# Kernel tuning notes

Measured on AMD Instinct MI355X. Metric: run time of the kernel, lower is better.

## Reference

```python
import jax, jax.numpy as jnp
import numpy as np

B, L = 32, 96
N = B * L
E = B * L * L
HID, LAT, EEMB = 128, 64, 32
NLAYERS = 3
LAMBDA_CONTRAST = 0.05


def _sinusoidal(t, dim):
    half = dim // 2
    freqs = jnp.exp(-jnp.log(10000.0) * jnp.arange(half, dtype=jnp.float32) / (half - 1))
    ang = t[:, None] * freqs[None, :]
    return jnp.concatenate([jnp.sin(ang), jnp.cos(ang)], axis=-1)


def _forward(H_0, X_0, H_1, X_1, cond_embedding, t_graph,
             Wi1, bi1, Wi2, bi2, Wi3, bi3, edge_table,
             We1, be1, We2, be2, Wx, Wh1, bh1, Wh2, bh2, Wout, bout,
             edges, chain_ids, generate_mask, lengths, shift):
    n = H_0.shape[0]
    b = lengths.shape[0]
    batch_ids = jnp.repeat(jnp.arange(b), lengths, total_repeat_length=n)
    t = t_graph[batch_ids]                      # (N,)
    mask = generate_mask
    mask_f = mask.astype(jnp.float32)

    # path interpolation
    tH = t[:, None]
    H_t = jnp.where(mask[:, None], (1.0 - tH) * H_0 + tH * H_1, H_1)
    X_t = jnp.where(mask[:, None], (1.0 - tH) * X_0 + tH * X_1, X_1)
    v_H_target = H_1 - H_0
    v_X_target = X_1 - X_0

    # edge types from chain-id masking (irregular gather)
    row, col = edges[0], edges[1]
    edge_types = (chain_ids[row] != chain_ids[col]).astype(jnp.int32)

    # --- velocity net ---
    t_embed = _sinusoidal(t, HID)
    h = jnp.concatenate([H_t, cond_embedding, t_embed], axis=-1)
    h = jax.nn.relu(h @ Wi1 + bi1)
    h = jax.nn.relu(h @ Wi2 + bi2)
    h = h @ Wi3 + bi3                            # (N, HID)
    eemb = edge_table[edge_types]                # (E, EEMB)

    X = X_t
    for l in range(NLAYERS):
        rel = X[row] - X[col]                    # (E, 3)
        d2 = jnp.sum(rel * rel, axis=-1, keepdims=True)
        ef = jnp.concatenate([h[row], h[col], d2, eemb], axis=-1)
        m = jax.nn.silu(ef @ We1[l] + be1[l])
        m = jax.nn.silu(m @ We2[l] + be2[l])     # (E, HID)
        coef = m @ Wx[l]                         # (E, 1)
        X = X + jax.ops.segment_sum(rel * coef, row, num_segments=n)
        agg = jax.ops.segment_sum(m, row, num_segments=n)
        hh = jnp.concatenate([h, agg], axis=-1)
        h = h + jax.nn.silu(hh @ Wh1[l] + bh1[l]) @ Wh2[l] + bh2[l]

    v_X_pred = jnp.where(mask[:, None], X, 0.0)
    v_H_pred = jnp.where(mask[:, None], h @ Wout + bout, 0.0)

    # --- losses ---
    msum = mask_f.sum() + 1e-8
    def masked_mse(pred, tgt):
        return (jnp.sum((pred - tgt) ** 2, axis=-1) * mask_f).sum() / msum
    loss_H_pos = masked_mse(v_H_pred, v_H_target)
    loss_X_pos = masked_mse(v_X_pred, v_X_target)

    # negatives: roll over node dim (matches torch indexing (arange+shift)%N)
    v_H_target_neg = jnp.roll(H_1, -shift, axis=0) - jnp.roll(H_0, -shift, axis=0)
    v_X_target_neg = jnp.roll(X_1, -shift, axis=0) - jnp.roll(X_0, -shift, axis=0)
    loss_H_neg = masked_mse(v_H_pred, v_H_target_neg)
    loss_X_neg = masked_mse(v_X_pred, v_X_target_neg)

    loss_H = loss_H_pos - LAMBDA_CONTRAST * loss_H_neg
    loss_X = loss_X_pos - LAMBDA_CONTRAST * loss_X_neg
    return jnp.stack([loss_H, loss_X, loss_H_pos, loss_X_pos, loss_H_neg, loss_X_neg])


def setup_inputs() -> dict:
    key = jax.random.key(0)
    ks = iter(jax.random.split(key, 40))
    def nrm(shape, fan_in):
        return jax.random.normal(next(ks), shape, dtype=jnp.float32) / np.sqrt(fan_in)

    # all-pairs edges within each graph (uniform lengths)
    idx = np.arange(L)
    rb, cb = np.repeat(idx, L), np.tile(idx, L)
    off = (np.arange(B) * L)[:, None]
    rows = (off + rb[None, :]).reshape(-1)
    cols = (off + cb[None, :]).reshape(-1)
    edges = jnp.asarray(np.stack([rows, cols]).astype(np.int32))

    d_in_mlp = LAT + 2 * HID       # 320
    d_in_e = 2 * HID + 1 + EEMB    # 289
    inp = {
        "H_0": jax.random.normal(next(ks), (N, LAT), dtype=jnp.float32),
        "X_0": jax.random.normal(next(ks), (N, 3), dtype=jnp.float32),
        "H_1": jax.random.normal(next(ks), (N, LAT), dtype=jnp.float32),
        "X_1": jax.random.normal(next(ks), (N, 3), dtype=jnp.float32),
        "cond_embedding": jax.random.normal(next(ks), (N, HID), dtype=jnp.float32),
        "t_graph": jax.random.uniform(next(ks), (B,), dtype=jnp.float32),
        "Wi1": nrm((d_in_mlp, HID), d_in_mlp), "bi1": jnp.zeros((HID,)),
        "Wi2": nrm((HID, HID), HID), "bi2": jnp.zeros((HID,)),
        "Wi3": nrm((HID, HID), HID), "bi3": jnp.zeros((HID,)),
        "edge_table": jax.random.normal(next(ks), (2, EEMB), dtype=jnp.float32),
        "We1": nrm((NLAYERS, d_in_e, HID), d_in_e), "be1": jnp.zeros((NLAYERS, HID)),
        "We2": nrm((NLAYERS, HID, HID), HID), "be2": jnp.zeros((NLAYERS, HID)),
        "Wx": nrm((NLAYERS, HID, 1), HID) * 0.01,
        "Wh1": nrm((NLAYERS, 2 * HID, HID), 2 * HID), "bh1": jnp.zeros((NLAYERS, HID)),
        "Wh2": nrm((NLAYERS, HID, HID), HID), "bh2": jnp.zeros((NLAYERS, HID)),
        "Wout": nrm((HID, LAT), HID), "bout": jnp.zeros((LAT,)),
        "edges": edges,
        "chain_ids": jax.random.randint(next(ks), (N,), 0, 3).astype(jnp.int32),
        "generate_mask": jax.random.bernoulli(next(ks), 0.5, (N,)),
        "lengths": jnp.full((B,), L, dtype=jnp.int32),
        "shift": 7,
    }
    return inp


def reference(H_0, X_0, H_1, X_1, cond_embedding, t_graph,
              Wi1, bi1, Wi2, bi2, Wi3, bi3, edge_table,
              We1, be1, We2, be2, Wx, Wh1, bh1, Wh2, bh2, Wout, bout,
              edges, chain_ids, generate_mask, lengths, shift):
    return _forward(H_0, X_0, H_1, X_1, cond_embedding, t_graph,
                    Wi1, bi1, Wi2, bi2, Wi3, bi3, edge_table,
                    We1, be1, We2, be2, Wx, Wh1, bh1, Wh2, bh2, Wout, bout,
                    edges, chain_ids, generate_mask, lengths, shift)
```

## Files before the change

### kernel.cpp

```cpp
#include <hip/hip_runtime.h>
#include <hip/hip_bf16.h>
#include <math.h>

#define NBATCH 32
#define LSEQ   96
#define NN     3072
#define HID    128
#define LAT    64
#define EEMB   32

#define OFF_H      0
#define OFF_X      (OFF_H   + NN*HID)
#define OFF_PA     (OFF_X   + NN*3)
#define OFF_AGG    (OFF_PA  + NN*HID)
#define OFF_DX     (OFF_AGG + NN*HID)
#define OFF_ET     (OFF_DX  + NN*3)
#define OFF_ACC    (OFF_ET  + 768)
#define OFF_NBID   (OFF_ACC + 8)
#define OFF_CUM    (OFF_NBID + NN)
#define OFF_PBH    (OFF_CUM + 40)
#define OFF_BPE    (OFF_PBH + NN*HID/2)
#define OFF_BAB    (OFF_BPE + 24576)
#define OFF_BH1    (OFF_BAB + 49152)
#define OFF_BH2    (OFF_BH1 + 49152)
#define OFF_BWO    (OFF_BH2 + 24576)
#define OFF_BWI1   (OFF_BWO + 4096)
#define OFF_BWI2   (OFF_BWI1 + 20480)
#define OFF_BWI3   (OFF_BWI2 + 8192)

typedef short bf16x8 __attribute__((ext_vector_type(8)));
typedef float f32x4  __attribute__((ext_vector_type(4)));

__device__ __forceinline__ short f2bf(float f) {
    unsigned u = __builtin_bit_cast(unsigned, f);
    unsigned r = (u + 0x7FFFu + ((u >> 16) & 1u)) >> 16;
    return (short)r;
}
__device__ __forceinline__ short2 f2bf2(float a, float b) {
    __hip_bfloat162 h = __float22bfloat162_rn(make_float2(a, b));
    short2 r;
    __builtin_memcpy(&r, &h, sizeof(r));
    return r;
}
__device__ __forceinline__ float bf2f(short s) {
    unsigned u = ((unsigned)(unsigned short)s) << 16;
    return __builtin_bit_cast(float, u);
}
__device__ __forceinline__ float silu(float z) {
    return z * __builtin_amdgcn_rcpf(1.0f + __expf(-z));
}

__global__ void k0a_prep(const float* __restrict__ edge_table,
                         const float* __restrict__ We1,
                         const int* __restrict__ lengths,
                         float* __restrict__ ws) {
    int* cum = (int*)(ws + OFF_CUM);
    int* nb  = (int*)(ws + OFF_NBID);
    float* et = ws + OFF_ET;
    int tid = threadIdx.x;
    if (tid == 0) {
        int s = 0;
        for (int b = 0; b < NBATCH; b++) { cum[b] = s; s += lengths[b]; }
        cum[NBATCH] = s;
    }
    if (tid < 8) ws[OFF_ACC + tid] = 0.0f;
    __syncthreads();
    for (int i = tid; i < NN; i += blockDim.x) {
        int b = NBATCH - 1;
        for (int q = 0; q < NBATCH; q++) { if (i < cum[q + 1]) { b = q; break; } }
        nb[i] = b;
    }
    for (int idx = tid; idx < 3 * 2 * HID; idx += blockDim.x) {
        int c = idx & 127;
        int t = (idx >> 7) & 1;
        int l = idx >> 8;
        const float* w = We1 + (l * 289 + 257) * HID + c;
        const float* e = edge_table + t * EEMB;
        float s = 0.f;
        for (int k = 0; k < EEMB; k++) s += e[k] * w[k * HID];
        et[idx] = s;
    }
}

__global__ void k0b_transpose(const float* __restrict__ We1, const float* __restrict__ We2,
                              const float* __restrict__ Wh1, const float* __restrict__ Wh2,
                              const float* __restrict__ Wout, const float* __restrict__ Wi1,
                              const float* __restrict__ Wi2, const float* __restrict__ Wi3,
                              float* __restrict__ ws) {
    int idx = blockIdx.x * 256 + threadIdx.x;
    short* bpe  = (short*)(ws + OFF_BPE);
    short* bab  = (short*)(ws + OFF_BAB);
    short* bh1  = (short*)(ws + OFF_BH1);
    short* bh2  = (short*)(ws + OFF_BH2);
    short* bwo  = (short*)(ws + OFF_BWO);
    short* bwi1 = (short*)(ws + OFF_BWI1);
    short* bwi2 = (short*)(ws + OFF_BWI2);
    short* bwi3 = (short*)(ws + OFF_BWI3);
    if (idx < 49152) {
        int k = idx & 127, n = (idx >> 7) & 127, l = idx >> 14;
        bpe[idx] = f2bf(We2[(l * 128 + k) * 128 + n]);
    } else if (idx < 147456) {
        int q = idx - 49152;
        int k = q & 127, n = (q >> 7) & 255, l = q >> 15;
        float v = (n < 128) ? We1[(l * 289 + k) * 128 + n]
                            : We1[(l * 289 + 128 + k) * 128 + (n - 128)];
        bab[q] = f2bf(v);
    } else if (idx < 245760) {
        int q = idx - 147456;
        int k = q & 255, n = (q >> 8) & 127, l = q >> 15;
        bh1[q] = f2bf(Wh1[(l * 256 + k) * 128 + n]);
    } else if (idx < 294912) {
        int q = idx - 245760;
        int k = q & 127, n = (q >> 7) & 127, l = q >> 14;
        bh2[q] = f2bf(Wh2[(l * 128 + k) * 128 + n]);
    } else if (idx < 303104) {
        int q = idx - 294912;
        int k = q & 127, n = q >> 7;
        bwo[q] = f2bf(Wout[k * 64 + n]);
    } else if (idx < 344064) {
        int q = idx - 303104;
        int n = q / 320, k = q - n * 320;
        bwi1[q] = f2bf(Wi1[k * 128 + n]);
    } else if (idx < 360448) {
        int q = idx - 344064;
        int k = q & 127, n = q >> 7;
        bwi2[q] = f2bf(Wi2[k * 128 + n]);
    } else if (idx < 376832) {
        int q = idx - 360448;
        int k = q & 127, n = q >> 7;
        bwi3[q] = f2bf(Wi3[k * 128 + n]);
    }
}

__global__ void __launch_bounds__(256)
k1s_node_init(const float* __restrict__ H0, const float* __restrict__ X0,
              const float* __restrict__ H1, const float* __restrict__ X1,
              const float* __restrict__ cond, const float* __restrict__ tg,
              const float* __restrict__ bi1, const float* __restrict__ bi2,
              const float* __restrict__ bi3, const float* __restrict__ be1,
              const int* __restrict__ gmask, float* __restrict__ ws) {
    __shared__ short u1[16 * 136];
    __shared__ short u2[16 * 136];
// ... 104 lines not shown
        #pragma unroll
        for (int i = 0; i < 2; i++) {
            int ct = 2 * w + i;
            bf16x8 bf = *(const bf16x8*)(bwi3 + (size_t)(16 * ct + lp) * 128 + kb);
            acc[i] = __builtin_amdgcn_mfma_f32_16x16x32_bf16(af, bf, acc[i], 0, 0, 0);
        }
    }
    #pragma unroll
    for (int i = 0; i < 2; i++) {
        int ch = 16 * (2 * w + i) + lp;
        float bb3 = bi3[ch];
        #pragma unroll
        for (int r = 0; r < 4; r++) {
            int row = quad * 4 + r;
            float h = acc[i][r] + bb3;
            ws[OFF_H + (size_t)(rowbase + row) * 128 + ch] = h;
            u1[row * 136 + ch] = f2bf(h);
        }
    }
    __syncthreads();

    f32x4 acc4[4];
    #pragma unroll
    for (int i = 0; i < 4; i++) acc4[i] = (f32x4){0.f, 0.f, 0.f, 0.f};
    #pragma unroll
    for (int s = 0; s < 4; s++) {
        int kb = s * 32 + quad * 8;
        bf16x8 af = *(const bf16x8*)(u1 + lp * 136 + kb);
        #pragma unroll
        for (int i = 0; i < 4; i++) {
            int ct4 = 4 * w + i;
            bf16x8 bf = *(const bf16x8*)(bab + (size_t)(16 * ct4 + lp) * 128 + kb);
            acc4[i] = __builtin_amdgcn_mfma_f32_16x16x32_bf16(af, bf, acc4[i], 0, 0, 0);
        }
    }
    short* pbh = (short*)(ws + OFF_PBH);
    #pragma unroll
    for (int i = 0; i < 4; i++) {
        int ct4 = 4 * w + i;
        #pragma unroll
        for (int r = 0; r < 4; r++) {
            int node = rowbase + quad * 4 + r;
            if (ct4 < 8) {
                int ch = 16 * ct4 + lp;
                ws[OFF_PA + (size_t)node * 128 + ch] = acc4[i][r] + be1[ch];
            } else {
                int ch = 16 * (ct4 - 8) + lp;
                pbh[(size_t)node * 128 + ch] = f2bf(acc4[i][r]);
            }
        }
    }
}

#define KG 4
__global__ void __launch_bounds__(384)
k3_edge(const float* __restrict__ We1, const float* __restrict__ Wx,
        const float* __restrict__ be2, const int* __restrict__ chain,
        int l, float* __restrict__ ws) {
    __shared__ short bS[128 * 136];
    __shared__ float pe0S[KG * 128], pe1S[KG * 128];
    __shared__ float d2S[KG * 96];
    __shared__ int   selS[KG * 96];
    __shared__ float xS[96 * 3];
    __shared__ float xT[KG * 3];
    __shared__ float wcS[128], wxS[128], be2S[128];
    __shared__ float aggP[6 * 128];
    __shared__ float coefS[96];

    int tid = threadIdx.x;
    int i0 = blockIdx.x * KG;
    int colbase = (i0 / 96) * 96;
    const float* Xc = ws + OFF_X;

    {
        const short* bpe = (const short*)(ws + OFF_BPE) + (size_t)l * 128 * 128;
        for (int idx = tid; idx < 2048; idx += 384) {
            int row = idx >> 4, c = idx & 15;
            *(bf16x8*)(bS + row * 136 + c * 8) = *(const bf16x8*)(bpe + row * 128 + c * 8);
        }
        if (tid < 288) xS[tid] = Xc[colbase * 3 + tid];
        if (tid < KG * 3) xT[tid] = Xc[(size_t)(i0 + tid / 3) * 3 + tid % 3];
    }
    __syncthreads();

    if (tid < 128) {
        #pragma unroll
        for (int g = 0; g < KG; g++) {
            float pav = ws[OFF_PA + (size_t)(i0 + g) * 128 + tid];
            pe0S[g * 128 + tid] = pav + ws[OFF_ET + l * 256 + tid];
            pe1S[g * 128 + tid] = pav + ws[OFF_ET + l * 256 + 128 + tid];
        }
    } else if (tid < 224) {
        int j = tid - 128;
        int cj = chain[colbase + j];
        #pragma unroll
        for (int g = 0; g < KG; g++) {
            float rx = xT[g * 3 + 0] - xS[j * 3 + 0];
            float ry = xT[g * 3 + 1] - xS[j * 3 + 1];
            float rz = xT[g * 3 + 2] - xS[j * 3 + 2];
            d2S[g * 96 + j]  = rx * rx + ry * ry + rz * rz;
            selS[g * 96 + j] = (chain[i0 + g] != cj) ? 1 : 0;
        }
    } else if (tid < 352) {
        int c = tid - 224;
        wcS[c]  = We1[(l * 289 + 256) * 128 + c];
        wxS[c]  = Wx[l * 128 + c];
        be2S[c] = be2[l * 128 + c];
    }

    int w = tid >> 6, lane = tid & 63;
    int quad = lane >> 4, lp = lane & 15;
    int jA = 16 * w + lp;
    const short* pbrow = (const short*)(ws + OFF_PBH) + (size_t)(colbase + jA) * 128;
    bf16x8 pbv[4];
    #pragma unroll
    for (int s = 0; s < 4; s++) pbv[s] = *(const bf16x8*)(pbrow + s * 32 + quad * 8);
    __syncthreads();

    for (int g = 0; g < KG; g++) {
        float d2j = d2S[g * 96 + jA];
        const float* peB = (selS[g * 96 + jA] ? pe1S : pe0S) + g * 128;

        f32x4 acc[8];
        #pragma unroll
        for (int t = 0; t < 8; t++) acc[t] = (f32x4){0.f, 0.f, 0.f, 0.f};

        #pragma unroll
        for (int s = 0; s < 4; s++) {
            int kb = s * 32 + quad * 8;
            float z[8];
            #pragma unroll
            for (int e = 0; e < 8; e++)
                z[e] = silu(peB[kb + e] + bf2f(pbv[s][e]) + d2j * wcS[kb + e]);
            bf16x8 af;
            #pragma unroll
            for (int e = 0; e < 8; e += 2) {
                short2 p = f2bf2(z[e], z[e + 1]);
                af[e] = p.x; af[e + 1] = p.y;
            }
            #pragma unroll
            for (int t = 0; t < 8; t++) {
                bf16x8 bf = *(const bf16x8*)(bS + (16 * t + lp) * 136 + kb);
                acc[t] = __builtin_amdgcn_mfma_f32_16x16x32_bf16(af, bf, acc[t], 0, 0, 0);
            }
        }

        float cp[4] = {0.f, 0.f, 0.f, 0.f};
        #pragma unroll
        for (int t = 0; t < 8; t++) {
            int ch = 16 * t + lp;
            float bb = be2S[ch];
            float wx = wxS[ch];
            float ag = 0.f;
            #pragma unroll
            for (int r = 0; r < 4; r++) {
                float m2 = silu(acc[t][r] + bb);
                ag += m2;
                cp[r] += m2 * wx;
            }
            ag += __shfl_xor(ag, 16);
            ag += __shfl_xor(ag, 32);
            if (lane < 16) aggP[w * 128 + ch] = ag;
        }
        #pragma unroll
        for (int r = 0; r < 4; r++) {
            float v = cp[r];
            v += __shfl_xor(v, 1);
            v += __shfl_xor(v, 2);
            v += __shfl_xor(v, 4);
            v += __shfl_xor(v, 8);
            if (lp == 0) coefS[16 * w + quad * 4 + r] = v;
        }
        __syncthreads();

        if (tid < 128) {
            float s = 0.f;
            #pragma unroll
            for (int q = 0; q < 6; q++) s += aggP[q * 128 + tid];
            ws[OFF_AGG + (size_t)(i0 + g) * 128 + tid] = s;
        }
        if (w < 3) {
            float v = (xT[g * 3 + w] - xS[lane * 3 + w]) * coefS[lane];
            if (lane < 32) v += (xT[g * 3 + w] - xS[(lane + 64) * 3 + w]) * coefS[lane + 64];
            #pragma unroll
            for (int o = 32; o > 0; o >>= 1) v += __shfl_down(v, o);
            if (lane == 0) ws[OFF_DX + (size_t)(i0 + g) * 3 + w] = v;
        }
        if (g < KG - 1) __syncthreads();
    }
}

__global__ void __launch_bounds__(256)
k4s_node_post(const float* __restrict__ bh1, const float* __restrict__ bh2,
              const float* __restrict__ be1, const float* __restrict__ bout,
              const float* __restrict__ H0, const float* __restrict__ X0,
              const float* __restrict__ H1, const float* __restrict__ X1,
              const int* __restrict__ gmask, const int* __restrict__ shiftp,
              int l, float* __restrict__ ws) {
    __shared__ short uS[16 * 136];
    __shared__ short hS[16 * 136];
    __shared__ float redE[4], redN[4];
    __shared__ float sxp, sxn, scnt;
    int rowbase = blockIdx.x * 96 + blockIdx.y * 16;
    int tid = threadIdx.x;
    int w = tid >> 6, lane = tid & 63;
    int quad = lane >> 4, lp = lane & 15;
    int nodeA = rowbase + lp;
    const short* b1 = (const short*)(ws + OFF_BH1) + (size_t)l * 128 * 256;
    const short* b2 = (const short*)(ws + OFF_BH2) + (size_t)l * 128 * 128;

    if (tid == 0) { sxp = 0.f; sxn = 0.f; scnt = 0.f; }
    if (tid < 48) {
        int node = rowbase + tid / 3, d = tid % 3;
        ws[OFF_X + (size_t)node * 3 + d] += ws[OFF_DX + (size_t)node * 3 + d];
    }

    f32x4 acc[2];
    acc[0] = (f32x4){0.f, 0.f, 0.f, 0.f};
    acc[1] = (f32x4){0.f, 0.f, 0.f, 0.f};
    #pragma unroll
    for (int s = 0; s < 8; s++) {
        int kb = s * 32 + quad * 8;
        const float* src = (kb < 128) ? (ws + OFF_H + (size_t)nodeA * 128 + kb)
                                      : (ws + OFF_AGG + (size_t)nodeA * 128 + (kb - 128));
        bf16x8 af;
        #pragma unroll
        for (int e = 0; e < 8; e += 2) {
            short2 p = f2bf2(src[e], src[e + 1]);
            af[e] = p.x; af[e + 1] = p.y;
        }
        #pragma unroll
        for (int i = 0; i < 2; i++) {
            int ct = 2 * w + i;
            bf16x8 bf = *(const bf16x8*)(b1 + (size_t)(16 * ct + lp) * 256 + kb);
            acc[i] = __builtin_amdgcn_mfma_f32_16x16x32_bf16(af, bf, acc[i], 0, 0, 0);
        }
    }
    #pragma unroll
    for (int i = 0; i < 2; i++) {
        int ch = 16 * (2 * w + i) + lp;
        float bb1 = bh1[l * 128 + ch];
        #pragma unroll
        for (int r = 0; r < 4; r++)
            uS[(quad * 4 + r) * 136 + ch] = f2bf(silu(acc[i][r] + bb1));
    }
    __syncthreads();

    acc[0] = (f32x4){0.f, 0.f, 0.f, 0.f};
    acc[1] = (f32x4){0.f, 0.f, 0.f, 0.f};
    #pragma unroll
    for (int s = 0; s < 4; s++) {
        int kb = s * 32 + quad * 8;
        bf16x8 af = *(const bf16x8*)(uS + lp * 136 + kb);
        #pragma unroll
        for (int i = 0; i < 2; i++) {
            int ct = 2 * w + i;
            bf16x8 bf = *(const bf16x8*)(b2 + (size_t)(16 * ct + lp) * 128 + kb);
            acc[i] = __builtin_amdgcn_mfma_f32_16x16x32_bf16(af, bf, acc[i], 0, 0, 0);
        }
    }
    #pragma unroll
    for (int i = 0; i < 2; i++) {
        int ch = 16 * (2 * w + i) + lp;
        float bb2 = bh2[l * 128 + ch];
        #pragma unroll
        for (int r = 0; r < 4; r++) {
            int row = quad * 4 + r;
            size_t off = OFF_H + (size_t)(rowbase + row) * 128 + ch;
            float h = ws[off] + acc[i][r] + bb2;
            ws[off] = h;
            hS[row * 136 + ch] = f2bf(h);
        }
    }
    __syncthreads();

    if (l < 2) {
        const short* bab = (const short*)(ws + OFF_BAB) + (size_t)(l + 1) * 256 * 128;
        f32x4 acc4[4];
        #pragma unroll
        for (int i = 0; i < 4; i++) acc4[i] = (f32x4){0.f, 0.f, 0.f, 0.f};
        #pragma unroll
        for (int s = 0; s < 4; s++) {
            int kb = s * 32 + quad * 8;
            bf16x8 af = *(const bf16x8*)(hS + lp * 136 + kb);
            #pragma unroll
            for (int i = 0; i < 4; i++) {
                int ct4 = 4 * w + i;
                bf16x8 bf = *(const bf16x8*)(bab + (size_t)(16 * ct4 + lp) * 128 + kb);
                acc4[i] = __builtin_amdgcn_mfma_f32_16x16x32_bf16(af, bf, acc4[i], 0, 0, 0);
            }
        }
        short* pbh = (short*)(ws + OFF_PBH);
        #pragma unroll
        for (int i = 0; i < 4; i++) {
            int ct4 = 4 * w + i;
            #pragma unroll
            for (int r = 0; r < 4; r++) {
                int node = rowbase + quad * 4 + r;
                if (ct4 < 8) {
                    int ch = 16 * ct4 + lp;
                    ws[OFF_PA + (size_t)node * 128 + ch] = acc4[i][r] + be1[(l + 1) * 128 + ch];
                } else {
                    int ch = 16 * (ct4 - 8) + lp;
                    pbh[(size_t)node * 128 + ch] = f2bf(acc4[i][r]);
                }
            }
        }
    } else {
        const short* bwo = (const short*)(ws + OFF_BWO);
        f32x4 accv = (f32x4){0.f, 0.f, 0.f, 0.f};
        #pragma unroll
        for (int s = 0; s < 4; s++) {
            int kb = s * 32 + quad * 8;
            bf16x8 af = *(const bf16x8*)(hS + lp * 136 + kb);
            bf16x8 bf = *(const bf16x8*)(bwo + (size_t)(16 * w + lp) * 128 + kb);
            accv = __builtin_amdgcn_mfma_f32_16x16x32_bf16(af, bf, accv, 0, 0, 0);
        }
        int s = shiftp[0] % NN; if (s < 0) s += NN;
        int col = 16 * w + lp;
        float bo = bout[col];
        float ep = 0.f, en = 0.f;
        #pragma unroll
        for (int r = 0; r < 4; r++) {
            int row = rowbase + quad * 4 + r;
            if (gmask[row] != 0) {
                int ip = row + s; if (ip >= NN) ip -= NN;
                float v  = accv[r] + bo;
                float tp = H1[(size_t)row * 64 + col] - H0[(size_t)row * 64 + col];
                float tn = H1[(size_t)ip * 64 + col]  - H0[(size_t)ip * 64 + col];
                float dp = v - tp, dn = v - tn;
                ep += dp * dp;
                en += dn * dn;
            }
        }
        #pragma unroll
        for (int o = 1; o < 64; o <<= 1) {
            ep += __shfl_xor(ep, o);
            en += __shfl_xor(en, o);
        }
        if (lane == 0) { redE[w] = ep; redN[w] = en; }

        if (tid < 16) {
            int node = rowbase + tid;
            if (gmask[node] != 0) {
                int ip = node + s; if (ip >= NN) ip -= NN;
                float xp = 0.f, xn = 0.f;
                #pragma unroll
                for (int d = 0; d < 3; d++) {
                    float xv  = ws[OFF_X + (size_t)node * 3 + d];
                    float tpx = X1[(size_t)node * 3 + d] - X0[(size_t)node * 3 + d];
                    float tnx = X1[(size_t)ip * 3 + d]   - X0[(size_t)ip * 3 + d];
                    xp += (xv - tpx) * (xv - tpx);
                    xn += (xv - tnx) * (xv - tnx);
                }
                atomicAdd(&sxp, xp);
                atomicAdd(&sxn, xn);
                atomicAdd(&scnt, 1.0f);
            }
        }
        __syncthreads();
        if (tid == 0) {
            float eT = redE[0] + redE[1] + redE[2] + redE[3];
            float nT = redN[0] + redN[1] + redN[2] + redN[3];
            float* acc0 = ws + OFF_ACC;
            atomicAdd(acc0 + 0, eT);
            atomicAdd(acc0 + 2, nT);
            atomicAdd(acc0 + 1, sxp);
            atomicAdd(acc0 + 3, sxn);
            atomicAdd(acc0 + 4, scnt);
        }
    }
}

__global__ void k6_final(const float* __restrict__ ws, float* __restrict__ out) {
    if (threadIdx.x == 0) {
        const float* acc = ws + OFF_ACC;
        float msum = acc[4] + 1e-8f;
        float lhp = acc[0] / msum, lxp = acc[1] / msum;
        float lhn = acc[2] / msum, lxn = acc[3] / msum;
        out[0] = lhp - 0.05f * lhn;
        out[1] = lxp - 0.05f * lxn;
        out[2] = lhp;
        out[3] = lxp;
        out[4] = lhn;
        out[5] = lxn;
    }
}

extern "C" void kernel_launch(void* const* d_in, const int* in_sizes, int n_in,
                              void* d_out, int out_size, void* d_ws, size_t ws_size,
                              hipStream_t stream) {
    (void)in_sizes; (void)n_in; (void)out_size; (void)ws_size;
    const float* H0   = (const float*)d_in[0];
    const float* X0   = (const float*)d_in[1];
    const float* H1   = (const float*)d_in[2];
    const float* X1   = (const float*)d_in[3];
    const float* cond = (const float*)d_in[4];
    const float* tg   = (const float*)d_in[5];
    const float* Wi1  = (const float*)d_in[6];
    const float* bi1  = (const float*)d_in[7];
    const float* Wi2  = (const float*)d_in[8];
    const float* bi2  = (const float*)d_in[9];
    const float* Wi3  = (const float*)d_in[10];
    const float* bi3  = (const float*)d_in[11];
    const float* etab = (const float*)d_in[12];
    const float* We1  = (const float*)d_in[13];
    const float* be1  = (const float*)d_in[14];
    const float* We2  = (const float*)d_in[15];
    const float* be2  = (const float*)d_in[16];
    const float* Wx   = (const float*)d_in[17];
    const float* Wh1  = (const float*)d_in[18];
    const float* bh1  = (const float*)d_in[19];
    const float* Wh2  = (const float*)d_in[20];
    const float* bh2  = (const float*)d_in[21];
    const float* Wout = (const float*)d_in[22];
    const float* bout = (const float*)d_in[23];
    const int* chain   = (const int*)d_in[25];
    const int* gmask   = (const int*)d_in[26];
    const int* lengths = (const int*)d_in[27];
    const int* shiftp  = (const int*)d_in[28];
    float* ws  = (float*)d_ws;
    float* out = (float*)d_out;

    k0a_prep<<<1, 256, 0, stream>>>(etab, We1, lengths, ws);
    k0b_transpose<<<1472, 256, 0, stream>>>(We1, We2, Wh1, Wh2, Wout, Wi1, Wi2, Wi3, ws);
    k1s_node_init<<<dim3(NBATCH, 6), 256, 0, stream>>>(H0, X0, H1, X1, cond, tg,
                                                       bi1, bi2, bi3, be1, gmask, ws);
    for (int l = 0; l < 3; l++) {
        k3_edge<<<NN / KG, 384, 0, stream>>>(We1, Wx, be2, chain, l, ws);
        k4s_node_post<<<dim3(NBATCH, 6), 256, 0, stream>>>(bh1, bh2, be1, bout,
                                                           H0, X0, H1, X1, gmask, shiftp, l, ws);
    }
    k6_final<<<1, 64, 0, stream>>>(ws, out);
}
```

Baseline: 390.5 us.

## Fuse node-update into edge kernel via last-block-done counter; merge prep kernels

Merges the two prep kernels into one launch and fuses the per-layer node post-processing into the edge kernel. Each of the 24 blocks covering a 96-node graph bumps a global counter, and the last one to finish runs the node MLP update for the whole graph. This removes three kernel launches and the gaps between them. In exchange, the node work runs on only 32 blocks placed at the tail of each edge launch, so it is less parallel, and the atomic counter and threadfences add synchronisation cost.

```diff
diff --git a/kernel.cpp b/kernel.cpp
--- a/kernel.cpp
+++ b/kernel.cpp
@@ -27,6 +27,7 @@
 #define OFF_BWI1   (OFF_BWO + 4096)
 #define OFF_BWI2   (OFF_BWI1 + 20480)
 #define OFF_BWI3   (OFF_BWI2 + 8192)
+#define OFF_CNT    (OFF_BWI3 + 8192)
 
 typedef short bf16x8 __attribute__((ext_vector_type(8)));
 typedef float f32x4  __attribute__((ext_vector_type(4)));
@@ -50,44 +51,43 @@
     return z * __builtin_amdgcn_rcpf(1.0f + __expf(-z));
 }
 
-__global__ void k0a_prep(const float* __restrict__ edge_table,
-                         const float* __restrict__ We1,
-                         const int* __restrict__ lengths,
-                         float* __restrict__ ws) {
-    int* cum = (int*)(ws + OFF_CUM);
-    int* nb  = (int*)(ws + OFF_NBID);
-    float* et = ws + OFF_ET;
+__global__ void k0_all(const float* __restrict__ edge_table, const float* __restrict__ We1,
+                       const int* __restrict__ lengths, const float* __restrict__ We2,
+                       const float* __restrict__ Wh1, const float* __restrict__ Wh2,
+                       const float* __restrict__ Wout, const float* __restrict__ Wi1,
+                       const float* __restrict__ Wi2, const float* __restrict__ Wi3,
+                       float* __restrict__ ws) {
     int tid = threadIdx.x;
-    if (tid == 0) {
-        int s = 0;
-        for (int b = 0; b < NBATCH; b++) { cum[b] = s; s += lengths[b]; }
-        cum[NBATCH] = s;
-    }
-    if (tid < 8) ws[OFF_ACC + tid] = 0.0f;
-    __syncthreads();
-    for (int i = tid; i < NN; i += blockDim.x) {
-        int b = NBATCH - 1;
-        for (int q = 0; q < NBATCH; q++) { if (i < cum[q + 1]) { b = q; break; } }
-        nb[i] = b;
-    }
-    for (int idx = tid; idx < 3 * 2 * HID; idx += blockDim.x) {
-        int c = idx & 127;
-        int t = (idx >> 7) & 1;
-        int l = idx >> 8;
-        const float* w = We1 + (l * 289 + 257) * HID + c;
-        const float* e = edge_table + t * EEMB;
-        float s = 0.f;
-        for (int k = 0; k < EEMB; k++) s += e[k] * w[k * HID];
-        et[idx] = s;
-    }
-}
-
-__global__ void k0b_transpose(const float* __restrict__ We1, const float* __restrict__ We2,
-                              const float* __restrict__ Wh1, const float* __restrict__ Wh2,
-                              const float* __restrict__ Wout, const float* __restrict__ Wi1,
-                              const float* __restrict__ Wi2, const float* __restrict__ Wi3,
-                              float* __restrict__ ws) {
-    int idx = blockIdx.x * 256 + threadIdx.x;
+    if (blockIdx.x == 1472) {
+        int* cum = (int*)(ws + OFF_CUM);
+        int* nb  = (int*)(ws + OFF_NBID);
+        float* et = ws + OFF_ET;
+        if (tid == 0) {
+            int s = 0;
+            for (int b = 0; b < NBATCH; b++) { cum[b] = s; s += lengths[b]; }
+            cum[NBATCH] = s;
+        }
+        if (tid < 8) ws[OFF_ACC + tid] = 0.0f;
+        if (tid < 96) ((unsigned*)(ws + OFF_CNT))[tid] = 0u;
+        __syncthreads();
+        for (int i = tid; i < NN; i += blockDim.x) {
+            int b = NBATCH - 1;
+            for (int q = 0; q < NBATCH; q++) { if (i < cum[q + 1]) { b = q; break; } }
+            nb[i] = b;
+        }
+        for (int idx = tid; idx < 3 * 2 * HID; idx += blockDim.x) {
+            int c = idx & 127;
+            int t = (idx >> 7) & 1;
+            int l = idx >> 8;
+            const float* w = We1 + (l * 289 + 257) * HID + c;
+            const float* e = edge_table + t * EEMB;
+            float s = 0.f;
+            for (int k = 0; k < EEMB; k++) s += e[k] * w[k * HID];
+            et[idx] = s;
+        }
+        return;
+    }
+    int idx = blockIdx.x * 256 + tid;
     short* bpe  = (short*)(ws + OFF_BPE);
     short* bab  = (short*)(ws + OFF_BAB);
     short* bh1  = (short*)(ws + OFF_BH1);
@@ -299,23 +299,47 @@
 }
 
 #define KG 4
-__global__ void __launch_bounds__(384)
-k3_edge(const float* __restrict__ We1, const float* __restrict__ Wx,
-        const float* __restrict__ be2, const int* __restrict__ chain,
-        int l, float* __restrict__ ws) {
-    __shared__ short bS[128 * 136];
-    __shared__ float pe0S[KG * 128], pe1S[KG * 128];
-    __shared__ float d2S[KG * 96];
-    __shared__ int   selS[KG * 96];
-    __shared__ float xS[96 * 3];
-    __shared__ float xT[KG * 3];
-    __shared__ float wcS[128], wxS[128], be2S[128];
-    __shared__ float aggP[6 * 128];
-    __shared__ float coefS[96];
+#define SM_BS    0
+#define SM_PE0   34816
+#define SM_PE1   36864
+#define SM_D2    38912
+#define SM_SEL   40448
+#define SM_XS    41984
+#define SM_XT    43136
+#define SM_WC    43200
+#define SM_WX    43712
+#define SM_BE2   44224
+#define SM_AGGP  44736
+#define SM_COEF  47808
+#define SM_FLAG  48192
+__global__ void __launch_bounds__(384, 5)
+k3f_edge(const float* __restrict__ We1, const float* __restrict__ Wx,
+         const float* __restrict__ be2, const int* __restrict__ chain,
+         const float* __restrict__ bh1, const float* __restrict__ bh2,
+         const float* __restrict__ be1, const float* __restrict__ bout,
+         const float* __restrict__ H0, const float* __restrict__ X0,
+         const float* __restrict__ H1, const float* __restrict__ X1,
+         const int* __restrict__ gmask, const int* __restrict__ shiftp,
+         int l, float* __restrict__ ws) {
+    __shared__ __align__(16) char smem[48256];
+    short* bS    = (short*)(smem + SM_BS);
+    float* pe0S  = (float*)(smem + SM_PE0);
+    float* pe1S  = (float*)(smem + SM_PE1);
+    float* d2S   = (float*)(smem + SM_D2);
+    int*   selS  = (int*)  (smem + SM_SEL);
+    float* xS    = (float*)(smem + SM_XS);
+    float* xT    = (float*)(smem + SM_XT);
+    float* wcS   = (float*)(smem + SM_WC);
+    float* wxS   = (float*)(smem + SM_WX);
+    float* be2S  = (float*)(smem + SM_BE2);
+    float* aggP  = (float*)(smem + SM_AGGP);
+    float* coefS = (float*)(smem + SM_COEF);
+    unsigned* flagS = (unsigned*)(smem + SM_FLAG);
 
     int tid = threadIdx.x;
     int i0 = blockIdx.x * KG;
-    int colbase = (i0 / 96) * 96;
+    int blk = i0 / 96;
+    int colbase = blk * 96;
     const float* Xc = ws + OFF_X;
 
     {
@@ -432,38 +456,36 @@
             for (int o = 32; o > 0; o >>= 1) v += __shfl_down(v, o);
             if (lane == 0) ws[OFF_DX + (size_t)(i0 + g) * 3 + w] = v;
         }
-        if (g < KG - 1) __syncthreads();
-    }
-}
-
-__global__ void __launch_bounds__(256)
-k4s_node_post(const float* __restrict__ bh1, const float* __restrict__ bh2,
-              const float* __restrict__ be1, const float* __restrict__ bout,
-              const float* __restrict__ H0, const float* __restrict__ X0,
-              const float* __restrict__ H1, const float* __restrict__ X1,
-              const int* __restrict__ gmask, const int* __restrict__ shiftp,
-              int l, float* __restrict__ ws) {
-    __shared__ short uS[16 * 136];
-    __shared__ short hS[16 * 136];
-    __shared__ float redE[4], redN[4];
-    __shared__ float sxp, sxn, scnt;
-    int rowbase = blockIdx.x * 96 + blockIdx.y * 16;
-    int tid = threadIdx.x;
-    int w = tid >> 6, lane = tid & 63;
-    int quad = lane >> 4, lp = lane & 15;
-    int nodeA = rowbase + lp;
+        __syncthreads();
+    }
+
+    if (tid == 0) {
+        __threadfence();
+        unsigned old = atomicAdd((unsigned*)(ws + OFF_CNT) + l * 32 + blk, 1u);
+        *flagS = old;
+    }
+    __syncthreads();
+    if (*flagS != 23u) return;
+    __threadfence();
+
+    short* uhS  = (short*)smem;
+    float* redE = (float*)(smem + 26112);
+    float* redN = (float*)(smem + 26136);
+    float* sx   = (float*)(smem + 26160);
+    __syncthreads();
+
+    if (tid == 0) { sx[0] = 0.f; sx[1] = 0.f; sx[2] = 0.f; }
+    if (tid < 288) {
+        int node = colbase + tid / 3, d = tid % 3;
+        ws[OFF_X + (size_t)node * 3 + d] += ws[OFF_DX + (size_t)node * 3 + d];
+    }
     const short* b1 = (const short*)(ws + OFF_BH1) + (size_t)l * 128 * 256;
     const short* b2 = (const short*)(ws + OFF_BH2) + (size_t)l * 128 * 128;
-
-    if (tid == 0) { sxp = 0.f; sxn = 0.f; scnt = 0.f; }
-    if (tid < 48) {
-        int node = rowbase + tid / 3, d = tid % 3;
-        ws[OFF_X + (size_t)node * 3 + d] += ws[OFF_DX + (size_t)node * 3 + d];
-    }
-
-    f32x4 acc[2];
-    acc[0] = (f32x4){0.f, 0.f, 0.f, 0.f};
-    acc[1] = (f32x4){0.f, 0.f, 0.f, 0.f};
+    int nodeA = colbase + 16 * w + lp;
+
+    f32x4 acc[8];
+    #pragma unroll
+    for (int t = 0; t < 8; t++) acc[t] = (f32x4){0.f, 0.f, 0.f, 0.f};
     #pragma unroll
     for (int s = 0; s < 8; s++) {
         int kb = s * 32 + quad * 8;
@@ -476,107 +498,124 @@
             af[e] = p.x; af[e + 1] = p.y;
         }
         #pragma unroll
-        for (int i = 0; i < 2; i++) {
-            int ct = 2 * w + i;
-            bf16x8 bf = *(const bf16x8*)(b1 + (size_t)(16 * ct + lp) * 256 + kb);
-            acc[i] = __builtin_amdgcn_mfma_f32_16x16x32_bf16(af, bf, acc[i], 0, 0, 0);
-        }
-    }
-    #pragma unroll
-    for (int i = 0; i < 2; i++) {
-        int ch = 16 * (2 * w + i) + lp;
+        for (int t = 0; t < 8; t++) {
+            bf16x8 bf = *(const bf16x8*)(b1 + (size_t)(16 * t + lp) * 256 + kb);
+            acc[t] = __builtin_amdgcn_mfma_f32_16x16x32_bf16(af, bf, acc[t], 0, 0, 0);
+        }
+    }
+    #pragma unroll
+    for (int t = 0; t < 8; t++) {
+        int ch = 16 * t + lp;
         float bb1 = bh1[l * 128 + ch];
         #pragma unroll
-        for (int r = 0; r < 4; r++)
-            uS[(quad * 4 + r) * 136 + ch] = f2bf(silu(acc[i][r] + bb1));
-    }
-    __syncthreads();
-
-    acc[0] = (f32x4){0.f, 0.f, 0.f, 0.f};
-    acc[1] = (f32x4){0.f, 0.f, 0.f, 0.f};
+        for (int r = 0; r < 4; r++) {
+            int row = 16 * w + quad * 4 + r;
+            uhS[row * 136 + ch] = f2bf(silu(acc[t][r] + bb1));
+        }
+    }
+    __syncthreads();
+
+    f32x4 acc2[8];
+    #pragma unroll
+    for (int t = 0; t < 8; t++) acc2[t] = (f32x4){0.f, 0.f, 0.f, 0.f};
     #pragma unroll
     for (int s = 0; s < 4; s++) {
         int kb = s * 32 + quad * 8;
-        bf16x8 af = *(const bf16x8*)(uS + lp * 136 + kb);
-        #pragma unroll
-        for (int i = 0; i < 2; i++) {
-            int ct = 2 * w + i;
-            bf16x8 bf = *(const bf16x8*)(b2 + (size_t)(16 * ct + lp) * 128 + kb);
-            acc[i] = __builtin_amdgcn_mfma_f32_16x16x32_bf16(af, bf, acc[i], 0, 0, 0);
-        }
-    }
-    #pragma unroll
-    for (int i = 0; i < 2; i++) {
-        int ch = 16 * (2 * w + i) + lp;
+        bf16x8 af = *(const bf16x8*)(uhS + (16 * w + lp) * 136 + kb);
+        #pragma unroll
+        for (int t = 0; t < 8; t++) {
+            bf16x8 bf = *(const bf16x8*)(b2 + (size_t)(16 * t + lp) * 128 + kb);
+            acc2[t] = __builtin_amdgcn_mfma_f32_16x16x32_bf16(af, bf, acc2[t], 0, 0, 0);
+        }
+    }
+    __syncthreads();
+    #pragma unroll
+    for (int t = 0; t < 8; t++) {
+        int ch = 16 * t + lp;
         float bb2 = bh2[l * 128 + ch];
         #pragma unroll
         for (int r = 0; r < 4; r++) {
-            int row = quad * 4 + r;
-            size_t off = OFF_H + (size_t)(rowbase + row) * 128 + ch;
-            float h = ws[off] + acc[i][r] + bb2;
+            int row = 16 * w + quad * 4 + r;
+            size_t off = OFF_H + (size_t)(colbase + row) * 128 + ch;
+            float h = ws[off] + acc2[t][r] + bb2;
             ws[off] = h;
-            hS[row * 136 + ch] = f2bf(h);
+            uhS[row * 136 + ch] = f2bf(h);
         }
     }
     __syncthreads();
 
     if (l < 2) {
         const short* bab = (const short*)(ws + OFF_BAB) + (size_t)(l + 1) * 256 * 128;
-        f32x4 acc4[4];
-        #pragma unroll
-        for (int i = 0; i < 4; i++) acc4[i] = (f32x4){0.f, 0.f, 0.f, 0.f};
+        short* pbh = (short*)(ws + OFF_PBH);
+        #pragma unroll
+        for (int half = 0; half < 2; half++) {
+            f32x4 acc4[8];
+            #pragma unroll
+            for (int i = 0; i < 8; i++) acc4[i] = (f32x4){0.f, 0.f, 0.f, 0.f};
+            #pragma unroll
+            for (int s = 0; s < 4; s++) {
+                int kb = s * 32 + quad * 8;
+                bf16x8 af = *(const bf16x8*)(uhS + (16 * w + lp) * 136 + kb);
+                #pragma unroll
+                for (int i = 0; i < 8; i++) {
+                    int ct = 8 * half + i;
+                    bf16x8 bf = *(const bf16x8*)(bab + (size_t)(16 * ct + lp) * 128 + kb);
+                    acc4[i] = __builtin_amdgcn_mfma_f32_16x16x32_bf16(af, bf, acc4[i], 0, 0, 0);
+                }
+            }
+            #pragma unroll
+            for (int i = 0; i < 8; i++) {
+                int ch = 16 * i + lp;
+                #pragma unroll
+                for (int r = 0; r < 4; r++) {
+                    int node = colbase + 16 * w + quad * 4 + r;
+                    if (half == 0)
+                        ws[OFF_PA + (size_t)node * 128 + ch] = acc4[i][r] + be1[(l + 1) * 128 + ch];
+                    else
+                        pbh[(size_t)node * 128 + ch] = f2bf(acc4[i][r]);
+                }
+            }
+        }
+    } else {
+        const short* bwo = (const short*)(ws + OFF_BWO);
+        f32x4 accv[4];
+        #pragma unroll
+        for (int t = 0; t < 4; t++) accv[t] = (f32x4){0.f, 0.f, 0.f, 0.f};
         #pragma unroll
         for (int s = 0; s < 4; s++) {
             int kb = s * 32 + quad * 8;
-            bf16x8 af = *(const bf16x8*)(hS + lp * 136 + kb);
-            #pragma unroll
-            for (int i = 0; i < 4; i++) {
-                int ct4 = 4 * w + i;
-                bf16x8 bf = *(const bf16x8*)(bab + (size_t)(16 * ct4 + lp) * 128 + kb);
-                acc4[i] = __builtin_amdgcn_mfma_f32_16x16x32_bf16(af, bf, acc4[i], 0, 0, 0);
-            }
-        }
-        short* pbh = (short*)(ws + OFF_PBH);
-        #pragma unroll
-        for (int i = 0; i < 4; i++) {
-            int ct4 = 4 * w + i;
+            bf16x8 af = *(const bf16x8*)(uhS + (16 * w + lp) * 136 + kb);
+            #pragma unroll
+            for (int t = 0; t < 4; t++) {
+                bf16x8 bf = *(const bf16x8*)(bwo + (size_t)(16 * t + lp) * 128 + kb);
+                accv[t] = __builtin_amdgcn_mfma_f32_16x16x32_bf16(af, bf, accv[t], 0, 0, 0);
+            }
+        }
+        int s = shiftp[0] % NN; if (s < 0) s += NN;
+        float mr[4]; int ipr[4]; int rowr[4];
+        #pragma unroll
+        for (int r = 0; r < 4; r++) {
+            int row = colbase + 16 * w + quad * 4 + r;
+            rowr[r] = row;
+            mr[r] = (gmask[row] != 0) ? 1.0f : 0.0f;
+            int ip = row + s; if (ip >= NN) ip -= NN;
+            ipr[r] = ip;
+        }
+        float ep = 0.f, en = 0.f;
+        #pragma unroll
+        for (int t = 0; t < 4; t++) {
+            int col = 16 * t + lp;
+            float bo = bout[col];
             #pragma unroll
             for (int r = 0; r < 4; r++) {
-                int node = rowbase + quad * 4 + r;
-                if (ct4 < 8) {
-                    int ch = 16 * ct4 + lp;
-                    ws[OFF_PA + (size_t)node * 128 + ch] = acc4[i][r] + be1[(l + 1) * 128 + ch];
-                } else {
-                    int ch = 16 * (ct4 - 8) + lp;
-                    pbh[(size_t)node * 128 + ch] = f2bf(acc4[i][r]);
+                if (mr[r] != 0.0f) {
+                    float v  = accv[t][r] + bo;
+                    float tp = H1[(size_t)rowr[r] * 64 + col] - H0[(size_t)rowr[r] * 64 + col];
+                    float tn = H1[(size_t)ipr[r] * 64 + col]  - H0[(size_t)ipr[r] * 64 + col];
+                    float dp = v - tp, dn = v - tn;
+                    ep += dp * dp;
+                    en += dn * dn;
                 }
-            }
-        }
-    } else {
-        const short* bwo = (const short*)(ws + OFF_BWO);
-        f32x4 accv = (f32x4){0.f, 0.f, 0.f, 0.f};
-        #pragma unroll
-        for (int s = 0; s < 4; s++) {
-            int kb = s * 32 + quad * 8;
-            bf16x8 af = *(const bf16x8*)(hS + lp * 136 + kb);
-            bf16x8 bf = *(const bf16x8*)(bwo + (size_t)(16 * w + lp) * 128 + kb);
-            accv = __builtin_amdgcn_mfma_f32_16x16x32_bf16(af, bf, accv, 0, 0, 0);
-        }
-        int s = shiftp[0] % NN; if (s < 0) s += NN;
-        int col = 16 * w + lp;
-        float bo = bout[col];
-        float ep = 0.f, en = 0.f;
-        #pragma unroll
-        for (int r = 0; r < 4; r++) {
-            int row = rowbase + quad * 4 + r;
-            if (gmask[row] != 0) {
-                int ip = row + s; if (ip >= NN) ip -= NN;
-                float v  = accv[r] + bo;
-                float tp = H1[(size_t)row * 64 + col] - H0[(size_t)row * 64 + col];
-                float tn = H1[(size_t)ip * 64 + col]  - H0[(size_t)ip * 64 + col];
-                float dp = v - tp, dn = v - tn;
-                ep += dp * dp;
-                en += dn * dn;
             }
         }
         #pragma unroll
@@ -586,8 +625,8 @@
         }
         if (lane == 0) { redE[w] = ep; redN[w] = en; }
 
-        if (tid < 16) {
-            int node = rowbase + tid;
+        if (tid < 96) {
+            int node = colbase + tid;
             if (gmask[node] != 0) {
                 int ip = node + s; if (ip >= NN) ip -= NN;
                 float xp = 0.f, xn = 0.f;
@@ -599,21 +638,22 @@
                     xp += (xv - tpx) * (xv - tpx);
                     xn += (xv - tnx) * (xv - tnx);
                 }
-                atomicAdd(&sxp, xp);
-                atomicAdd(&sxn, xn);
-                atomicAdd(&scnt, 1.0f);
+                atomicAdd(&sx[0], xp);
+                atomicAdd(&sx[1], xn);
+                atomicAdd(&sx[2], 1.0f);
             }
         }
         __syncthreads();
         if (tid == 0) {
-            float eT = redE[0] + redE[1] + redE[2] + redE[3];
-            float nT = redN[0] + redN[1] + redN[2] + redN[3];
+            float eT = 0.f, nT = 0.f;
+            #pragma unroll
+            for (int g = 0; g < 6; g++) { eT += redE[g]; nT += redN[g]; }
             float* acc0 = ws + OFF_ACC;
             atomicAdd(acc0 + 0, eT);
             atomicAdd(acc0 + 2, nT);
-            atomicAdd(acc0 + 1, sxp);
-            atomicAdd(acc0 + 3, sxn);
-            atomicAdd(acc0 + 4, scnt);
+            atomicAdd(acc0 + 1, sx[0]);
+            atomicAdd(acc0 + 3, sx[1]);
+            atomicAdd(acc0 + 4, sx[2]);
         }
     }
 }
@@ -668,14 +708,14 @@
     float* ws  = (float*)d_ws;
     float* out = (float*)d_out;
 
-    k0a_prep<<<1, 256, 0, stream>>>(etab, We1, lengths, ws);
-    k0b_transpose<<<1472, 256, 0, stream>>>(We1, We2, Wh1, Wh2, Wout, Wi1, Wi2, Wi3, ws);
+    k0_all<<<1473, 256, 0, stream>>>(etab, We1, lengths, We2, Wh1, Wh2,
+                                     Wout, Wi1, Wi2, Wi3, ws);
     k1s_node_init<<<dim3(NBATCH, 6), 256, 0, stream>>>(H0, X0, H1, X1, cond, tg,
                                                        bi1, bi2, bi3, be1, gmask, ws);
     for (int l = 0; l < 3; l++) {
-        k3_edge<<<NN / KG, 384, 0, stream>>>(We1, Wx, be2, chain, l, ws);
-        k4s_node_post<<<dim3(NBATCH, 6), 256, 0, stream>>>(bh1, bh2, be1, bout,
-                                                           H0, X0, H1, X1, gmask, shiftp, l, ws);
+        k3f_edge<<<NN / KG, 384, 0, stream>>>(We1, Wx, be2, chain,
+                                              bh1, bh2, be1, bout,
+                                              H0, X0, H1, X1, gmask, shiftp, l, ws);
     }
     k6_final<<<1, 64, 0, stream>>>(ws, out);
 }
```

After: 738.3 us. 1.89x slower.

## Restructure edge kernel to one wave per target node, merge prep kernels

Applied to the files above, without the earlier changes.

The edge kernel now gives each of its 4 waves its own target node and loops over all 96 source rows in tiles of 16. It keeps the aggregation and coordinate-update partial sums in registers, so the shared-memory reductions and per-target block barriers go away. It also reads PA, the edge-type bias and the source-row bf16 features directly per tile instead of staging them, and it drops the block size from 384 to 256 threads. Separately, the two setup kernels are fused into one launch by adding an extra block. The trade-offs are more redundant global or L2 loads of PA and the source rows per wave, and longer serial per-wave loops.

```diff
diff --git a/kernel.cpp b/kernel.cpp
--- a/kernel.cpp
+++ b/kernel.cpp
@@ -27,6 +27,7 @@
 #define OFF_BWI1   (OFF_BWO + 4096)
 #define OFF_BWI2   (OFF_BWI1 + 20480)
 #define OFF_BWI3   (OFF_BWI2 + 8192)
+#define OFF_CNT    (OFF_BWI3 + 8192)
 
 typedef short bf16x8 __attribute__((ext_vector_type(8)));
 typedef float f32x4  __attribute__((ext_vector_type(4)));
@@ -50,44 +51,42 @@
     return z * __builtin_amdgcn_rcpf(1.0f + __expf(-z));
 }
 
-__global__ void k0a_prep(const float* __restrict__ edge_table,
-                         const float* __restrict__ We1,
-                         const int* __restrict__ lengths,
-                         float* __restrict__ ws) {
-    int* cum = (int*)(ws + OFF_CUM);
-    int* nb  = (int*)(ws + OFF_NBID);
-    float* et = ws + OFF_ET;
+__global__ void k0_all(const float* __restrict__ edge_table, const float* __restrict__ We1,
+                       const int* __restrict__ lengths, const float* __restrict__ We2,
+                       const float* __restrict__ Wh1, const float* __restrict__ Wh2,
+                       const float* __restrict__ Wout, const float* __restrict__ Wi1,
+                       const float* __restrict__ Wi2, const float* __restrict__ Wi3,
+                       float* __restrict__ ws) {
     int tid = threadIdx.x;
-    if (tid == 0) {
-        int s = 0;
-        for (int b = 0; b < NBATCH; b++) { cum[b] = s; s += lengths[b]; }
-        cum[NBATCH] = s;
-    }
-    if (tid < 8) ws[OFF_ACC + tid] = 0.0f;
-    __syncthreads();
-    for (int i = tid; i < NN; i += blockDim.x) {
-        int b = NBATCH - 1;
-        for (int q = 0; q < NBATCH; q++) { if (i < cum[q + 1]) { b = q; break; } }
-        nb[i] = b;
-    }
-    for (int idx = tid; idx < 3 * 2 * HID; idx += blockDim.x) {
-        int c = idx & 127;
-        int t = (idx >> 7) & 1;
-        int l = idx >> 8;
-        const float* w = We1 + (l * 289 + 257) * HID + c;
-        const float* e = edge_table + t * EEMB;
-        float s = 0.f;
-        for (int k = 0; k < EEMB; k++) s += e[k] * w[k * HID];
-        et[idx] = s;
-    }
-}
-
-__global__ void k0b_transpose(const float* __restrict__ We1, const float* __restrict__ We2,
-                              const float* __restrict__ Wh1, const float* __restrict__ Wh2,
-                              const float* __restrict__ Wout, const float* __restrict__ Wi1,
-                              const float* __restrict__ Wi2, const float* __restrict__ Wi3,
-                              float* __restrict__ ws) {
-    int idx = blockIdx.x * 256 + threadIdx.x;
+    if (blockIdx.x == 1472) {
+        int* cum = (int*)(ws + OFF_CUM);
+        int* nb  = (int*)(ws + OFF_NBID);
+        float* et = ws + OFF_ET;
+        if (tid == 0) {
+            int s = 0;
+            for (int b = 0; b < NBATCH; b++) { cum[b] = s; s += lengths[b]; }
+            cum[NBATCH] = s;
+        }
+        if (tid < 8) ws[OFF_ACC + tid] = 0.0f;
+        __syncthreads();
+        for (int i = tid; i < NN; i += blockDim.x) {
+            int b = NBATCH - 1;
+            for (int q = 0; q < NBATCH; q++) { if (i < cum[q + 1]) { b = q; break; } }
+            nb[i] = b;
+        }
+        for (int idx = tid; idx < 3 * 2 * HID; idx += blockDim.x) {
+            int c = idx & 127;
+            int t = (idx >> 7) & 1;
+            int l = idx >> 8;
+            const float* w = We1 + (l * 289 + 257) * HID + c;
+            const float* e = edge_table + t * EEMB;
+            float s = 0.f;
+            for (int k = 0; k < EEMB; k++) s += e[k] * w[k * HID];
+            et[idx] = s;
+        }
+        return;
+    }
+    int idx = blockIdx.x * 256 + tid;
     short* bpe  = (short*)(ws + OFF_BPE);
     short* bab  = (short*)(ws + OFF_BAB);
     short* bh1  = (short*)(ws + OFF_BH1);
@@ -298,74 +297,61 @@
     }
 }
 
-#define KG 4
-__global__ void __launch_bounds__(384)
-k3_edge(const float* __restrict__ We1, const float* __restrict__ Wx,
-        const float* __restrict__ be2, const int* __restrict__ chain,
-        int l, float* __restrict__ ws) {
+#define KGW 4
+__global__ void __launch_bounds__(256)
+k3w_edge(const float* __restrict__ We1, const float* __restrict__ Wx,
+         const float* __restrict__ be2, const int* __restrict__ chain,
+         int l, float* __restrict__ ws) {
     __shared__ short bS[128 * 136];
-    __shared__ float pe0S[KG * 128], pe1S[KG * 128];
-    __shared__ float d2S[KG * 96];
-    __shared__ int   selS[KG * 96];
     __shared__ float xS[96 * 3];
-    __shared__ float xT[KG * 3];
-    __shared__ float wcS[128], wxS[128], be2S[128];
-    __shared__ float aggP[6 * 128];
-    __shared__ float coefS[96];
+    __shared__ int   cS[96];
+    __shared__ float wcS[128], wxS[128], be2S[128], et0S[128], et1S[128];
 
     int tid = threadIdx.x;
-    int i0 = blockIdx.x * KG;
+    int i0 = blockIdx.x * KGW;
     int colbase = (i0 / 96) * 96;
     const float* Xc = ws + OFF_X;
 
     {
         const short* bpe = (const short*)(ws + OFF_BPE) + (size_t)l * 128 * 128;
-        for (int idx = tid; idx < 2048; idx += 384) {
+        for (int idx = tid; idx < 2048; idx += 256) {
             int row = idx >> 4, c = idx & 15;
             *(bf16x8*)(bS + row * 136 + c * 8) = *(const bf16x8*)(bpe + row * 128 + c * 8);
         }
-        if (tid < 288) xS[tid] = Xc[colbase * 3 + tid];
-        if (tid < KG * 3) xT[tid] = Xc[(size_t)(i0 + tid / 3) * 3 + tid % 3];
+        for (int q = tid; q < 288; q += 256) xS[q] = Xc[colbase * 3 + q];
+        if (tid < 96) cS[tid] = chain[colbase + tid];
+        if (tid < 128) {
+            wcS[tid]  = We1[(l * 289 + 256) * 128 + tid];
+            wxS[tid]  = Wx[l * 128 + tid];
+            be2S[tid] = be2[l * 128 + tid];
+            et0S[tid] = ws[OFF_ET + l * 256 + tid];
+            et1S[tid] = ws[OFF_ET + l * 256 + 128 + tid];
+        }
     }
     __syncthreads();
-
-    if (tid < 128) {
-        #pragma unroll
-        for (int g = 0; g < KG; g++) {
-            float pav = ws[OFF_PA + (size_t)(i0 + g) * 128 + tid];
-            pe0S[g * 128 + tid] = pav + ws[OFF_ET + l * 256 + tid];
-            pe1S[g * 128 + tid] = pav + ws[OFF_ET + l * 256 + 128 + tid];
-        }
-    } else if (tid < 224) {
-        int j = tid - 128;
-        int cj = chain[colbase + j];
-        #pragma unroll
-        for (int g = 0; g < KG; g++) {
-            float rx = xT[g * 3 + 0] - xS[j * 3 + 0];
-            float ry = xT[g * 3 + 1] - xS[j * 3 + 1];
-            float rz = xT[g * 3 + 2] - xS[j * 3 + 2];
-            d2S[g * 96 + j]  = rx * rx + ry * ry + rz * rz;
-            selS[g * 96 + j] = (chain[i0 + g] != cj) ? 1 : 0;
-        }
-    } else if (tid < 352) {
-        int c = tid - 224;
-        wcS[c]  = We1[(l * 289 + 256) * 128 + c];
-        wxS[c]  = Wx[l * 128 + c];
-        be2S[c] = be2[l * 128 + c];
-    }
 
     int w = tid >> 6, lane = tid & 63;
     int quad = lane >> 4, lp = lane & 15;
-    int jA = 16 * w + lp;
-    const short* pbrow = (const short*)(ws + OFF_PBH) + (size_t)(colbase + jA) * 128;
-    bf16x8 pbv[4];
-    #pragma unroll
-    for (int s = 0; s < 4; s++) pbv[s] = *(const bf16x8*)(pbrow + s * 32 + quad * 8);
-    __syncthreads();
-
-    for (int g = 0; g < KG; g++) {
-        float d2j = d2S[g * 96 + jA];
-        const float* peB = (selS[g * 96 + jA] ? pe1S : pe0S) + g * 128;
+    int tgt = i0 + w;
+    int jt = tgt - colbase;
+    float xt0 = xS[jt * 3 + 0], xt1 = xS[jt * 3 + 1], xt2 = xS[jt * 3 + 2];
+    int ct = cS[jt];
+    const float* paP = ws + OFF_PA + (size_t)tgt * 128;
+    const short* pbh = (const short*)(ws + OFF_PBH);
+
+    float agg8[8];
+    #pragma unroll
+    for (int t = 0; t < 8; t++) agg8[t] = 0.f;
+    float dxp0 = 0.f, dxp1 = 0.f, dxp2 = 0.f;
+
+    for (int T = 0; T < 6; T++) {
+        int row = T * 16 + lp;
+        float rx = xt0 - xS[row * 3 + 0];
+        float ry = xt1 - xS[row * 3 + 1];
+        float rz = xt2 - xS[row * 3 + 2];
+        float d2 = rx * rx + ry * ry + rz * rz;
+        bool sel = (cS[row] != ct);
+        const short* pbrow = pbh + (size_t)(colbase + row) * 128;
 
         f32x4 acc[8];
         #pragma unroll
@@ -374,14 +360,15 @@
         #pragma unroll
         for (int s = 0; s < 4; s++) {
             int kb = s * 32 + quad * 8;
-            float z[8];
-            #pragma unroll
-            for (int e = 0; e < 8; e++)
-                z[e] = silu(peB[kb + e] + bf2f(pbv[s][e]) + d2j * wcS[kb + e]);
+            bf16x8 pbv = *(const bf16x8*)(pbrow + kb);
             bf16x8 af;
             #pragma unroll
             for (int e = 0; e < 8; e += 2) {
-                short2 p = f2bf2(z[e], z[e + 1]);
+                float et0a = sel ? et1S[kb + e]     : et0S[kb + e];
+                float et0b = sel ? et1S[kb + e + 1] : et0S[kb + e + 1];
+                float za = silu(paP[kb + e]     + et0a + bf2f(pbv[e])     + d2 * wcS[kb + e]);
+                float zb = silu(paP[kb + e + 1] + et0b + bf2f(pbv[e + 1]) + d2 * wcS[kb + e + 1]);
+                short2 p = f2bf2(za, zb);
                 af[e] = p.x; af[e + 1] = p.y;
             }
             #pragma unroll
@@ -397,42 +384,47 @@
             int ch = 16 * t + lp;
             float bb = be2S[ch];
             float wx = wxS[ch];
-            float ag = 0.f;
             #pragma unroll
             for (int r = 0; r < 4; r++) {
                 float m2 = silu(acc[t][r] + bb);
-                ag += m2;
+                agg8[t] += m2;
                 cp[r] += m2 * wx;
             }
-            ag += __shfl_xor(ag, 16);
-            ag += __shfl_xor(ag, 32);
-            if (lane < 16) aggP[w * 128 + ch] = ag;
         }
         #pragma unroll
         for (int r = 0; r < 4; r++) {
-            float v = cp[r];
-            v += __shfl_xor(v, 1);
-            v += __shfl_xor(v, 2);
-            v += __shfl_xor(v, 4);
-            v += __shfl_xor(v, 8);
-            if (lp == 0) coefS[16 * w + quad * 4 + r] = v;
-        }
-        __syncthreads();
-
-        if (tid < 128) {
-            float s = 0.f;
-            #pragma unroll
-            for (int q = 0; q < 6; q++) s += aggP[q * 128 + tid];
-            ws[OFF_AGG + (size_t)(i0 + g) * 128 + tid] = s;
-        }
-        if (w < 3) {
-            float v = (xT[g * 3 + w] - xS[lane * 3 + w]) * coefS[lane];
-            if (lane < 32) v += (xT[g * 3 + w] - xS[(lane + 64) * 3 + w]) * coefS[lane + 64];
-            #pragma unroll
-            for (int o = 32; o > 0; o >>= 1) v += __shfl_down(v, o);
-            if (lane == 0) ws[OFF_DX + (size_t)(i0 + g) * 3 + w] = v;
-        }
-        if (g < KG - 1) __syncthreads();
+            cp[r] += __shfl_xor(cp[r], 1);
+            cp[r] += __shfl_xor(cp[r], 2);
+            cp[r] += __shfl_xor(cp[r], 4);
+            cp[r] += __shfl_xor(cp[r], 8);
+        }
+        #pragma unroll
+        for (int r = 0; r < 4; r++) {
+            int rr = T * 16 + quad * 4 + r;
+            dxp0 += cp[r] * (xt0 - xS[rr * 3 + 0]);
+            dxp1 += cp[r] * (xt1 - xS[rr * 3 + 1]);
+            dxp2 += cp[r] * (xt2 - xS[rr * 3 + 2]);
+        }
+    }
+
+    #pragma unroll
+    for (int t = 0; t < 8; t++) {
+        agg8[t] += __shfl_xor(agg8[t], 16);
+        agg8[t] += __shfl_xor(agg8[t], 32);
+    }
+    dxp0 += __shfl_xor(dxp0, 16); dxp0 += __shfl_xor(dxp0, 32);
+    dxp1 += __shfl_xor(dxp1, 16); dxp1 += __shfl_xor(dxp1, 32);
+    dxp2 += __shfl_xor(dxp2, 16); dxp2 += __shfl_xor(dxp2, 32);
+
+    if (lane < 16) {
+        #pragma unroll
+        for (int t = 0; t < 8; t++)
+            ws[OFF_AGG + (size_t)tgt * 128 + 16 * t + lp] = agg8[t];
+    }
+    if (lane == 0) {
+        ws[OFF_DX + (size_t)tgt * 3 + 0] = dxp0;
+        ws[OFF_DX + (size_t)tgt * 3 + 1] = dxp1;
+        ws[OFF_DX + (size_t)tgt * 3 + 2] = dxp2;
     }
 }
 
@@ -668,12 +660,12 @@
     float* ws  = (float*)d_ws;
     float* out = (float*)d_out;
 
-    k0a_prep<<<1, 256, 0, stream>>>(etab, We1, lengths, ws);
-    k0b_transpose<<<1472, 256, 0, stream>>>(We1, We2, Wh1, Wh2, Wout, Wi1, Wi2, Wi3, ws);
+    k0_all<<<1473, 256, 0, stream>>>(etab, We1, lengths, We2, Wh1, Wh2,
+                                     Wout, Wi1, Wi2, Wi3, ws);
     k1s_node_init<<<dim3(NBATCH, 6), 256, 0, stream>>>(H0, X0, H1, X1, cond, tg,
                                                        bi1, bi2, bi3, be1, gmask, ws);
     for (int l = 0; l < 3; l++) {
-        k3_edge<<<NN / KG, 384, 0, stream>>>(We1, Wx, be2, chain, l, ws);
+        k3w_edge<<<NN / KGW, 256, 0, stream>>>(We1, Wx, be2, chain, l, ws);
         k4s_node_post<<<dim3(NBATCH, 6), 256, 0, stream>>>(bh1, bh2, be1, bout,
                                                            H0, X0, H1, X1, gmask, shiftp, l, ws);
     }
```

After: 397.2 us. Within noise of the previous version (+1.7%).
